# Kernel optimization log

Hardware: AMD Instinct MI355X
Metric: run time of the kernel (lower is better)

Reference implementation:

```python
import jax, jax.numpy as jnp
import numpy as np

NUM_HEADS = 16

def setup_inputs() -> dict:
    key = jax.random.key(0)
    ks = jax.random.split(key, 7)
    B, Q, K, D = 4, 512, 4096, 1024
    return {
        'query':  jax.random.normal(ks[0], (B, Q, D), dtype=jnp.float32),
        'memory': jax.random.normal(ks[1], (B, K, D), dtype=jnp.float32),
        'bias':   jax.random.normal(ks[2], (B, K), dtype=jnp.float32),
        'Wq': jax.random.normal(ks[3], (D, D), dtype=jnp.float32) * (D ** -0.5),
        'Wk': jax.random.normal(ks[4], (D, D), dtype=jnp.float32) * (D ** -0.5),
        'Wv': jax.random.normal(ks[5], (D, D), dtype=jnp.float32) * (D ** -0.5),
        'Wo': jax.random.normal(ks[6], (D, D), dtype=jnp.float32) * (D ** -0.5),
    }

def reference(query, memory, bias, Wq, Wk, Wv, Wo):
    B, Qn, _ = query.shape
    _, Kn, _ = memory.shape
    H = NUM_HEADS
    E = Wq.shape[1]
    dh = E // H
    scale = dh ** -0.5
    # projections (bias-free linears), split heads: [B, H, len, dh]
    q = (query @ Wq).reshape(B, Qn, H, dh).transpose(0, 2, 1, 3)
    k = (memory @ Wk).reshape(B, Kn, H, dh).transpose(0, 2, 1, 3)
    v = (memory @ Wv).reshape(B, Kn, H, dh).transpose(0, 2, 1, 3)
    scores = jnp.einsum('bhqd,bhkd->bhqk', q, k) * scale
    scores = scores + bias[:, None, None, :]          # additive support bias over K
    weights = jax.nn.softmax(scores, axis=-1)          # dropout p=0.0 -> identity
    out = jnp.einsum('bhqk,bhkd->bhqd', weights, v)
    out = out.transpose(0, 2, 1, 3).reshape(B, Qn, E)
    return out @ Wo
```

## Files before the change

### kernel.cpp

```cpp
#include <hip/hip_runtime.h>

typedef __attribute__((ext_vector_type(8))) short bf16x8;
typedef __attribute__((ext_vector_type(4))) short bf16x4;
typedef __attribute__((ext_vector_type(4))) float f32x4;

#define MFMA32(a,b,c) __builtin_amdgcn_mfma_f32_16x16x32_bf16((a),(b),(c),0,0,0)
#define MFMA16(a,b,c) __builtin_amdgcn_mfma_f32_16x16x16bf16_1k((a),(b),(c),0,0,0)
#define LOG2E 1.44269504f

#define BAR() asm volatile("s_barrier" ::: "memory")
#define VMW_(n) asm volatile("s_waitcnt vmcnt(" #n ")" ::: "memory")
#define VMW(n) VMW_(n)

__device__ __forceinline__ unsigned short f2bf(float f) {
  unsigned int u = __float_as_uint(f);
  u += 0x7fffu + ((u >> 16) & 1u);
  return (unsigned short)(u >> 16);
}

__device__ __forceinline__ void cp16(const void* g, void* l) {
  __builtin_amdgcn_global_load_lds((const __attribute__((address_space(1))) void*)g,
                                   (__attribute__((address_space(3))) void*)l, 16, 0, 0);
}

__global__ void conv_both(const float* __restrict__ q, const float* __restrict__ m,
                          const float* __restrict__ bias,
                          unsigned short* __restrict__ qo, unsigned short* __restrict__ mo,
                          float* __restrict__ bz) {
  int i = blockIdx.x * 256 + threadIdx.x;
  if (i < 524288) {
    float4 v = ((const float4*)q)[i];
    ushort4 o; o.x = f2bf(v.x); o.y = f2bf(v.y); o.z = f2bf(v.z); o.w = f2bf(v.w);
    ((ushort4*)qo)[i] = o;
  } else if (i < 4718592) {
    int j = i - 524288;
    float4 v = ((const float4*)m)[j];
    ushort4 o; o.x = f2bf(v.x); o.y = f2bf(v.y); o.z = f2bf(v.z); o.w = f2bf(v.w);
    ((ushort4*)mo)[j] = o;
  } else {
    int j = i - 4718592;
    float4 v = ((const float4*)bias)[j];
    float4 o;
    o.x = __builtin_fmaf(v.x, LOG2E, -16.f);
    o.y = __builtin_fmaf(v.y, LOG2E, -16.f);
    o.z = __builtin_fmaf(v.z, LOG2E, -16.f);
    o.w = __builtin_fmaf(v.w, LOG2E, -16.f);
    ((float4*)bz)[j] = o;
  }
}

__global__ void transpose4(const float* __restrict__ Wq, const float* __restrict__ Wk,
                           const float* __restrict__ Wv, const float* __restrict__ Wo,
                           unsigned short* __restrict__ dst) {
  __shared__ float t[32][33];
  int z = blockIdx.z;
  const float* W = (z == 0) ? Wq : (z == 1) ? Wk : (z == 2) ? Wv : Wo;
  unsigned short* WT = dst + (size_t)z * 1048576;
  int bx = blockIdx.x * 32, by = blockIdx.y * 32;
  int x = threadIdx.x, y0 = threadIdx.y;
#pragma unroll
  for (int r = 0; r < 4; ++r)
    t[y0 + r * 8][x] = W[(size_t)(by + y0 + r * 8) * 1024 + bx + x];
  __syncthreads();
#pragma unroll
  for (int r = 0; r < 4; ++r)
    WT[(size_t)(bx + y0 + r * 8) * 1024 + by + x] = f2bf(t[x][y0 + r * 8]);
}

__global__ __launch_bounds__(512, 2) void gemm_kv(
    const unsigned short* __restrict__ A,
    const unsigned short* __restrict__ Bk,
    const unsigned short* __restrict__ Bv,
    unsigned short* __restrict__ Kp,
    unsigned short* __restrict__ Vt)
{
  __shared__ __attribute__((aligned(16))) unsigned short lds[65536];
  const int tid = threadIdx.x;
  const int w = tid >> 6, lane = tid & 63;
  const int lh = lane & 15, q4 = lane >> 4;
  const int id = blockIdx.x;
  const int xcd = id & 7, j = id >> 3;
  const int tm = (xcd * 8 + (j >> 3)) * 256;
  const int tn = (j & 7) * 128;
  const int wm = (w >> 1) * 64, wn = (w & 1) * 64;

  const int r8 = lane >> 3;
  const int scol = ((lane & 7) ^ r8) * 8;
  const int srow = w * 8 + r8;
  const int fs0 = ((0 + q4) ^ (lh & 7)) * 8;
  const int fs1 = ((4 + q4) ^ (lh & 7)) * 8;

  const unsigned short* Ag = A  + (size_t)tm * 1024 + scol;
  const unsigned short* Kg = Bk + (size_t)tn * 1024 + scol;
  const unsigned short* Vg = Bv + (size_t)tn * 1024 + scol;

#define STG_A(BUF,KT,I) cp16(Ag + (size_t)((I)*64 + srow) * 1024 + (KT)*64, \
                             lds + (BUF)*32768 + (I)*4096 + w*512)
#define STG_K(BUF,KT,I) cp16(Kg + (size_t)((I)*64 + srow) * 1024 + (KT)*64, \
                             lds + (BUF)*32768 + 16384 + (I)*4096 + w*512)
#define STG_V(BUF,KT,I) cp16(Vg + (size_t)((I)*64 + srow) * 1024 + (KT)*64, \
                             lds + (BUF)*32768 + 24576 + (I)*4096 + w*512)

  f32x4 acck[4][4] = {}, accv[4][4] = {};
  bf16x8 aE[4], aO[4], bP[4], bQ[4];

  STG_A(0, 0, 0); STG_A(0, 0, 1); STG_A(0, 0, 2); STG_A(0, 0, 3);
  STG_K(0, 0, 0); STG_K(0, 0, 1);
  STG_V(0, 0, 0); STG_V(0, 0, 1);
  STG_A(1, 1, 0); STG_A(1, 1, 1); STG_A(1, 1, 2); STG_A(1, 1, 3);
  VMW(6);
  BAR();
#pragma unroll
  for (int m = 0; m < 4; ++m)
    aE[m] = *(const bf16x8*)(lds + (wm + m * 16 + lh) * 64 + fs0);
#pragma unroll
  for (int n = 0; n < 4; ++n)
    bP[n] = *(const bf16x8*)(lds + 16384 + (wn + n * 16 + lh) * 64 + fs0);

#define KV_TILE(CURB, TP1, TP2, DO_SB, DO_SA, VM1N, VM3N, DO_V3, DO_RDN)      \
  {                                                                           \
    const unsigned short* bse = lds + (CURB) * 32768;                         \
    const unsigned short* bnx = lds + ((CURB) ^ 1) * 32768;                   \
    const int nx = (CURB) ^ 1;                                                \
                            \
    BAR();                                                                    \
    _Pragma("unroll") for (int m = 0; m < 4; ++m)                             \
      aO[m] = *(const bf16x8*)(bse + (wm + m * 16 + lh) * 64 + fs1);          \
    _Pragma("unroll") for (int n = 0; n < 4; ++n)                             \
      bQ[n] = *(const bf16x8*)(bse + 16384 + (wn + n * 16 + lh) * 64 + fs1);  \
    if (DO_SB) { STG_K(nx, TP1, 0); STG_K(nx, TP1, 1); }                      \
    __builtin_amdgcn_s_setprio(1);                                            \
    _Pragma("unroll") for (int m = 0; m < 4; ++m)                             \
      _Pragma("unroll") for (int n = 0; n < 4; ++n)                           \
        acck[m][n] = MFMA32(aE[m], bP[n], acck[m][n]);                        \
    __builtin_amdgcn_s_setprio(0);                                            \
                      \
    VMW(VM1N);                                                                \
    BAR();                                                                    \
    _Pragma("unroll") for (int n = 0; n < 4; ++n)                             \
      bP[n] = *(const bf16x8*)(bse + 24576 + (wn + n * 16 + lh) * 64 + fs0);  \
    if (DO_SB) { STG_V(nx, TP1, 0); STG_V(nx, TP1, 1); }                      \
    __builtin_amdgcn_s_setprio(1);                                            \
    _Pragma("unroll") for (int m = 0; m < 4; ++m)                             \
      _Pragma("unroll") for (int n = 0; n < 4; ++n)                           \
        acck[m][n] = MFMA32(aO[m], bQ[n], acck[m][n]);                        \
    __builtin_amdgcn_s_setprio(0);                                            \
                         \
    BAR();                                                                    \
    _Pragma("unroll") for (int n = 0; n < 4; ++n)                             \
      bQ[n] = *(const bf16x8*)(bse + 24576 + (wn + n * 16 + lh) * 64 + fs1);  \
    if (DO_SA) { STG_A(CURB, TP2, 0); STG_A(CURB, TP2, 1); }                  \
    __builtin_amdgcn_s_setprio(1);                                            \
    _Pragma("unroll") for (int m = 0; m < 4; ++m)                             \
      _Pragma("unroll") for (int n = 0; n < 4; ++n)                           \
        accv[m][n] = MFMA32(aE[m], bP[n], accv[m][n]);                        \
    __builtin_amdgcn_s_setprio(0);                                            \
                   \
    if (DO_V3) { VMW(VM3N); }                                                 \
    BAR();                                                                    \
    if (DO_RDN) {                                                             \
      _Pragma("unroll") for (int m = 0; m < 4; ++m)                           \
        aE[m] = *(const bf16x8*)(bnx + (wm + m * 16 + lh) * 64 + fs0);        \
      _Pragma("unroll") for (int n = 0; n < 4; ++n)                           \
        bP[n] = *(const bf16x8*)(bnx + 16384 + (wn + n * 16 + lh) * 64 + fs0);\
    }                                                                         \
    if (DO_SA) { STG_A(CURB, TP2, 2); STG_A(CURB, TP2, 3); }                  \
    __builtin_amdgcn_s_setprio(1);                                            \
    _Pragma("unroll") for (int m = 0; m < 4; ++m)                             \
      _Pragma("unroll") for (int n = 0; n < 4; ++n)                           \
        accv[m][n] = MFMA32(aO[m], bQ[n], accv[m][n]);                        \
    __builtin_amdgcn_s_setprio(0);                                            \
  }

  for (int t = 0; t < 14; ++t) {
    KV_TILE(t & 1, t + 1, t + 2, 1, 1, 6, 4, 1, 1);
  }
  KV_TILE(0, 15, 16, 1, 0, 6, 2, 1, 1);
  KV_TILE(1, 16, 17, 0, 0, 0, 0, 0, 0);

#undef KV_TILE
#undef STG_A
#undef STG_K
#undef STG_V

#pragma unroll
  for (int m = 0; m < 4; ++m)
#pragma unroll
    for (int n = 0; n < 4; ++n) {
      int row = tm + wm + m * 16 + q4 * 4;
      int col = tn + wn + n * 16 + lh;
#pragma unroll
      for (int e = 0; e < 4; ++e)
        Kp[(size_t)(row + e) * 1024 + col] = f2bf(acck[m][n][e]);
    }

  __syncthreads();
#pragma unroll
  for (int m = 0; m < 4; ++m)
#pragma unroll
    for (int n = 0; n < 4; ++n) {
      int row = wm + m * 16 + q4 * 4;
      int col = wn + n * 16 + lh;
      ushort4 v4;
      v4.x = f2bf(accv[m][n][0]); v4.y = f2bf(accv[m][n][1]);
      v4.z = f2bf(accv[m][n][2]); v4.w = f2bf(accv[m][n][3]);
      *(ushort4*)(lds + col * 256 + (row ^ ((col & 31) << 3))) = v4;
    }
  __syncthreads();
#pragma unroll
  for (int p = 0; p < 8; ++p) {
    int col = p * 16 + (tid >> 5);
    int jb = tid & 31;
    const unsigned short* src = lds + col * 256 + ((jb ^ (col & 31)) << 3);
    *(int4*)(Vt + (size_t)(tn + col) * 16384 + tm + jb * 8) = *(const int4*)src;
  }
}

__global__ __launch_bounds__(256) void gemm_bt64(
    const unsigned short* __restrict__ A, const unsigned short* __restrict__ B,
    float* __restrict__ Cf, unsigned short* __restrict__ Cb,
    int M, int N, int K, float scale)
{
  __shared__ __attribute__((aligned(16))) unsigned short lds[6144];
  int w = threadIdx.x >> 6, lane = threadIdx.x & 63;
  int lh = lane & 15, q4 = lane >> 4;
  int tm = blockIdx.y * 128, tn = blockIdx.x * 64;
  int wm = (w & 1) * 64, wn = (w >> 1) * 32;

  int srow = lane >> 2;
  int scol = ((lane & 3) ^ ((lane >> 3) & 3)) << 3;
  int q4s = (q4 ^ ((lh >> 1) & 3)) << 3;

  f32x4 acc[4][2] = {};

  for (int k0 = 0; k0 < K; k0 += 32) {
#pragma unroll
    for (int i = 0; i < 2; ++i) {
      int c = w * 2 + i;
      int row = c * 16 + srow;
      cp16(A + (size_t)(tm + row) * K + k0 + scol, lds + c * 512);
    }
    {
      int row = w * 16 + srow;
      cp16(B + (size_t)(tn + row) * K + k0 + scol, lds + 4096 + w * 512);
    }
    __syncthreads();
    bf16x8 afr[4], bfr[2];
#pragma unroll
    for (int r = 0; r < 4; ++r)
      afr[r] = *(const bf16x8*)(lds + (wm + r * 16 + lh) * 32 + q4s);
#pragma unroll
    for (int c = 0; c < 2; ++c)
      bfr[c] = *(const bf16x8*)(lds + 4096 + (wn + c * 16 + lh) * 32 + q4s);
#pragma unroll
    for (int r = 0; r < 4; ++r)
#pragma unroll
      for (int c = 0; c < 2; ++c)
        acc[r][c] = MFMA32(afr[r], bfr[c], acc[r][c]);
    __syncthreads();
  }

#pragma unroll
  for (int r = 0; r < 4; ++r)
#pragma unroll
    for (int c = 0; c < 2; ++c)
#pragma unroll
      for (int e = 0; e < 4; ++e) {
        int row = tm + wm + r * 16 + q4 * 4 + e;
        int col = tn + wn + c * 16 + lh;
        if (Cb) Cb[(size_t)row * N + col] = f2bf(acc[r][c][e] * scale);
        else    Cf[(size_t)row * N + col] = acc[r][c][e] * scale;
      }
}

__global__ __launch_bounds__(256) void attn_kernel(
    const unsigned short* __restrict__ Q, const unsigned short* __restrict__ Kp,
    const unsigned short* __restrict__ VT, const float* __restrict__ bz,
    float* __restrict__ po, float* __restrict__ lp)
{
  __shared__ __attribute__((aligned(16))) unsigned short Klds[4096];
  __shared__ __attribute__((aligned(16))) unsigned short Vlds[4096];
  int w = threadIdx.x >> 6, lane = threadIdx.x & 63;
  int lh = lane & 15, q4 = lane >> 4;

  int id = blockIdx.x;
  int xcd = id & 7, j = id >> 3;
  int ql = j & 7;
  int half = ql & 1, qt = ql >> 1;
  int bh = (j >> 3) * 8 + xcd;
  int b = bh >> 4, h = bh & 15;
  int q0 = qt * 128;
  int t00 = half * 2048;

  const unsigned short* Qb = Q + (size_t)(b * 512 + q0 + w * 32) * 1024 + h * 64;
  const unsigned short* Kb = Kp + (size_t)(b * 4096) * 1024 + h * 64;
  const unsigned short* Vb = VT + (size_t)(h * 64) * 16384 + b * 4096;
  const float* bzg = bz + (size_t)b * 4096;

  bf16x8 bq[2][2];
#pragma unroll
  for (int s = 0; s < 2; ++s)
#pragma unroll
    for (int th = 0; th < 2; ++th)
      bq[s][th] = *(const bf16x8*)(Qb + (size_t)(s * 16 + lh) * 1024 + th * 32 + q4 * 8);

  f32x4 oa[2][4] = {};
  float ls[2] = {0.f, 0.f};

  int rl = lane >> 3, blk = lane & 7;
  int sw = ((blk ^ rl) * 8);

  for (int ti = 0; ti < 32; ++ti) {
    int t = t00 + ti * 64;
#pragma unroll
    for (int r = 0; r < 2; ++r) {
      int seg = r * 4 + w;
      int row = seg * 8 + rl;
      cp16(Kb + (size_t)(t + row) * 1024 + sw, Klds + seg * 512);
      cp16(Vb + (size_t)row * 16384 + t + sw, Vlds + seg * 512);
    }
    __syncthreads();

    float4 bz4[4];
#pragma unroll
    for (int c = 0; c < 4; ++c)
      bz4[c] = *(const float4*)(bzg + t + c * 16 + q4 * 4);

    bf16x8 kf[4][2];
#pragma unroll
    for (int c = 0; c < 4; ++c)
#pragma unroll
      for (int th = 0; th < 2; ++th)
        kf[c][th] = *(const bf16x8*)(Klds + (c * 16 + lh) * 64 + (((th << 2) + q4) ^ (lh & 7)) * 8);
    bf16x4 vf[4][4];
#pragma unroll
    for (int c = 0; c < 4; ++c)
#pragma unroll
      for (int c2 = 0; c2 < 4; ++c2)
        vf[c][c2] = *(const bf16x4*)(Vlds + (c2 * 16 + lh) * 64 +
                                     (((c << 1) + (q4 >> 1)) ^ (lh & 7)) * 8 + (q4 & 1) * 4);

#pragma unroll
    for (int s = 0; s < 2; ++s) {
#pragma unroll
      for (int c = 0; c < 4; ++c) {
        f32x4 z = {};
        z = MFMA32(kf[c][0], bq[s][0], z);
        z = MFMA32(kf[c][1], bq[s][1], z);
        float bzf[4] = {bz4[c].x, bz4[c].y, bz4[c].z, bz4[c].w};
        bf16x4 pb;
        float ps = 0.f;
#pragma unroll
        for (int e = 0; e < 4; ++e) {
          float p = __builtin_amdgcn_exp2f(z[e] + bzf[e]);
          ps += p;
          pb[e] = (short)f2bf(p);
        }
        ls[s] += ps;
#pragma unroll
        for (int c2 = 0; c2 < 4; ++c2)
          oa[s][c2] = MFMA16(vf[c][c2], pb, oa[s][c2]);
      }
    }
    __syncthreads();
  }

#pragma unroll
  for (int s = 0; s < 2; ++s) {
    ls[s] += __shfl_xor(ls[s], 16);
    ls[s] += __shfl_xor(ls[s], 32);
  }

  int sl = bh * 4 + qt;
  float* pslice = po + (size_t)(half * 256 + sl) * 8192;
#pragma unroll
  for (int s = 0; s < 2; ++s) {
    if (q4 == 0) lp[half * 32768 + sl * 128 + w * 32 + s * 16 + lh] = ls[s];
#pragma unroll
    for (int c2 = 0; c2 < 4; ++c2)
#pragma unroll
      for (int e = 0; e < 4; ++e)
        pslice[(c2 * 16 + q4 * 4 + e) * 128 + w * 32 + s * 16 + lh] = oa[s][c2][e];
  }
}

__global__ void norm_kernel(const float* __restrict__ po, const float* __restrict__ lp,
                            unsigned short* __restrict__ ao) {
  int g = blockIdx.x * 256 + threadIdx.x;
  int d8 = (g & 7) * 8;
  int rowid = g >> 3;
  int bh = rowid >> 9, rq = rowid & 511, qt = rq >> 7, qcol = rq & 127;
  int sl = bh * 4 + qt;
  const float* p0 = po + (size_t)sl * 8192;
  const float* p1 = po + (size_t)(256 + sl) * 8192;
  float l = lp[sl * 128 + qcol] + lp[32768 + sl * 128 + qcol];
  float inv = 1.f / l;
  unsigned short o8[8];
#pragma unroll
  for (int k = 0; k < 8; ++k)
    o8[k] = f2bf((p0[(d8 + k) * 128 + qcol] + p1[(d8 + k) * 128 + qcol]) * inv);
  int b = bh >> 4, h = bh & 15;
  unsigned short* dst = ao + (size_t)(b * 512 + qt * 128 + qcol) * 1024 + h * 64 + d8;
  *(ushort4*)dst = *(ushort4*)o8;
  *(ushort4*)(dst + 4) = *(ushort4*)(o8 + 4);
}

extern "C" void kernel_launch(void* const* d_in, const int* in_sizes, int n_in,
                              void* d_out, int out_size, void* d_ws, size_t ws_size,
                              hipStream_t stream) {
  const float* query  = (const float*)d_in[0];
  const float* memory = (const float*)d_in[1];
  const float* bias   = (const float*)d_in[2];
  const float* Wq     = (const float*)d_in[3];
  const float* Wk     = (const float*)d_in[4];
  const float* Wv     = (const float*)d_in[5];
  const float* Wo     = (const float*)d_in[6];
  float* out = (float*)d_out;

  unsigned short* ws  = (unsigned short*)d_ws;
  unsigned short* qbf = ws;
  unsigned short* mbf = qbf + 2097152;
  unsigned short* WqT = mbf + 16777216;
  unsigned short* WkT = WqT + 1048576;
  unsigned short* WvT = WkT + 1048576;
  unsigned short* WoT = WvT + 1048576;
  unsigned short* qp  = WoT + 1048576;
  unsigned short* kp  = qp + 2097152;
  unsigned short* vT  = kp + 16777216;
  unsigned short* ao  = vT + 16777216;
  float* bzw = (float*)(ao + 2097152);
  float* po = (float*)ws;
  float* lp = po + 4194304;

  conv_both<<<18448, 256, 0, stream>>>(query, memory, bias, qbf, mbf, bzw);
  transpose4<<<dim3(32, 32, 4), dim3(32, 8), 0, stream>>>(Wq, Wk, Wv, Wo, WqT);

  gemm_bt64<<<dim3(16, 16), 256, 0, stream>>>(qbf, WqT, nullptr, qp, 2048, 1024, 1024, 0.125f * LOG2E);
  gemm_kv<<<512, 512, 0, stream>>>(mbf, WkT, WvT, kp, vT);

  attn_kernel<<<512, 256, 0, stream>>>(qp, kp, vT, bzw, po, lp);
  norm_kernel<<<1024, 256, 0, stream>>>(po, lp, ao);

  gemm_bt64<<<dim3(16, 16), 256, 0, stream>>>(ao, WoT, out, nullptr, 2048, 1024, 1024, 1.f);
}
```

Baseline: 304.4 us.

## Double-buffer gemm_bt64 and simplify the KV projection pipeline to one barrier per tile

The output/Q projection GEMM gets a second LDS buffer. The next K-slice is now prefetched right after a single barrier at the top of each step, so the trailing barrier goes away and loads overlap the MFMAs. The KV projection kernel drops its hand-staggered macro schedule, with its split loads, custom waitcnts and raw s_barrier. In its place is a plain double-buffered loop that loads the whole next tile, then runs the K and V MFMAs in two k-halves. This is simpler, but the generic __syncthreads may wait on all outstanding loads, which could expose memory latency the old finer-grained schedule hid.

Measured after the change: 289.7 us. -4.8%, faster.

```diff
diff --git a/kernel.cpp b/kernel.cpp
--- a/kernel.cpp
+++ b/kernel.cpp
@@ -7,10 +7,6 @@
 #define MFMA32(a,b,c) __builtin_amdgcn_mfma_f32_16x16x32_bf16((a),(b),(c),0,0,0)
 #define MFMA16(a,b,c) __builtin_amdgcn_mfma_f32_16x16x16bf16_1k((a),(b),(c),0,0,0)
 #define LOG2E 1.44269504f
-
-#define BAR() asm volatile("s_barrier" ::: "memory")
-#define VMW_(n) asm volatile("s_waitcnt vmcnt(" #n ")" ::: "memory")
-#define VMW(n) VMW_(n)
 
 __device__ __forceinline__ unsigned short f2bf(float f) {
   unsigned int u = __float_as_uint(f);
@@ -102,83 +98,63 @@
                              lds + (BUF)*32768 + 24576 + (I)*4096 + w*512)
 
   f32x4 acck[4][4] = {}, accv[4][4] = {};
-  bf16x8 aE[4], aO[4], bP[4], bQ[4];
 
   STG_A(0, 0, 0); STG_A(0, 0, 1); STG_A(0, 0, 2); STG_A(0, 0, 3);
   STG_K(0, 0, 0); STG_K(0, 0, 1);
   STG_V(0, 0, 0); STG_V(0, 0, 1);
-  STG_A(1, 1, 0); STG_A(1, 1, 1); STG_A(1, 1, 2); STG_A(1, 1, 3);
-  VMW(6);
-  BAR();
-#pragma unroll
-  for (int m = 0; m < 4; ++m)
-    aE[m] = *(const bf16x8*)(lds + (wm + m * 16 + lh) * 64 + fs0);
-#pragma unroll
-  for (int n = 0; n < 4; ++n)
-    bP[n] = *(const bf16x8*)(lds + 16384 + (wn + n * 16 + lh) * 64 + fs0);
-
-#define KV_TILE(CURB, TP1, TP2, DO_SB, DO_SA, VM1N, VM3N, DO_V3, DO_RDN)      \
-  {                                                                           \
-    const unsigned short* bse = lds + (CURB) * 32768;                         \
-    const unsigned short* bnx = lds + ((CURB) ^ 1) * 32768;                   \
-    const int nx = (CURB) ^ 1;                                                \
-                            \
-    BAR();                                                                    \
-    _Pragma("unroll") for (int m = 0; m < 4; ++m)                             \
-      aO[m] = *(const bf16x8*)(bse + (wm + m * 16 + lh) * 64 + fs1);          \
-    _Pragma("unroll") for (int n = 0; n < 4; ++n)                             \
-      bQ[n] = *(const bf16x8*)(bse + 16384 + (wn + n * 16 + lh) * 64 + fs1);  \
-    if (DO_SB) { STG_K(nx, TP1, 0); STG_K(nx, TP1, 1); }                      \
-    __builtin_amdgcn_s_setprio(1);                                            \
-    _Pragma("unroll") for (int m = 0; m < 4; ++m)                             \
-      _Pragma("unroll") for (int n = 0; n < 4; ++n)                           \
-        acck[m][n] = MFMA32(aE[m], bP[n], acck[m][n]);                        \
-    __builtin_amdgcn_s_setprio(0);                                            \
-                      \
-    VMW(VM1N);                                                                \
-    BAR();                                                                    \
-    _Pragma("unroll") for (int n = 0; n < 4; ++n)                             \
-      bP[n] = *(const bf16x8*)(bse + 24576 + (wn + n * 16 + lh) * 64 + fs0);  \
-    if (DO_SB) { STG_V(nx, TP1, 0); STG_V(nx, TP1, 1); }                      \
-    __builtin_amdgcn_s_setprio(1);                                            \
-    _Pragma("unroll") for (int m = 0; m < 4; ++m)                             \
-      _Pragma("unroll") for (int n = 0; n < 4; ++n)                           \
-        acck[m][n] = MFMA32(aO[m], bQ[n], acck[m][n]);                        \
-    __builtin_amdgcn_s_setprio(0);                                            \
-                         \
-    BAR();                                                                    \
-    _Pragma("unroll") for (int n = 0; n < 4; ++n)                             \
-      bQ[n] = *(const bf16x8*)(bse + 24576 + (wn + n * 16 + lh) * 64 + fs1);  \
-    if (DO_SA) { STG_A(CURB, TP2, 0); STG_A(CURB, TP2, 1); }                  \
-    __builtin_amdgcn_s_setprio(1);                                            \
-    _Pragma("unroll") for (int m = 0; m < 4; ++m)                             \
-      _Pragma("unroll") for (int n = 0; n < 4; ++n)                           \
-        accv[m][n] = MFMA32(aE[m], bP[n], accv[m][n]);                        \
-    __builtin_amdgcn_s_setprio(0);                                            \
-                   \
-    if (DO_V3) { VMW(VM3N); }                                                 \
-    BAR();                                                                    \
-    if (DO_RDN) {                                                             \
-      _Pragma("unroll") for (int m = 0; m < 4; ++m)                           \
-        aE[m] = *(const bf16x8*)(bnx + (wm + m * 16 + lh) * 64 + fs0);        \
-      _Pragma("unroll") for (int n = 0; n < 4; ++n)                           \
-        bP[n] = *(const bf16x8*)(bnx + 16384 + (wn + n * 16 + lh) * 64 + fs0);\
-    }                                                                         \
-    if (DO_SA) { STG_A(CURB, TP2, 2); STG_A(CURB, TP2, 3); }                  \
-    __builtin_amdgcn_s_setprio(1);                                            \
-    _Pragma("unroll") for (int m = 0; m < 4; ++m)                             \
-      _Pragma("unroll") for (int n = 0; n < 4; ++n)                           \
-        accv[m][n] = MFMA32(aO[m], bQ[n], accv[m][n]);                        \
-    __builtin_amdgcn_s_setprio(0);                                            \
-  }
-
-  for (int t = 0; t < 14; ++t) {
-    KV_TILE(t & 1, t + 1, t + 2, 1, 1, 6, 4, 1, 1);
-  }
-  KV_TILE(0, 15, 16, 1, 0, 6, 2, 1, 1);
-  KV_TILE(1, 16, 17, 0, 0, 0, 0, 0, 0);
-
-#undef KV_TILE
+
+  for (int t = 0; t < 16; ++t) {
+    const unsigned short* bse = lds + (t & 1) * 32768;
+    const int nx = (t & 1) ^ 1;
+    __syncthreads();
+    if (t < 15) {
+      STG_A(nx, t + 1, 0); STG_A(nx, t + 1, 1);
+      STG_A(nx, t + 1, 2); STG_A(nx, t + 1, 3);
+      STG_K(nx, t + 1, 0); STG_K(nx, t + 1, 1);
+      STG_V(nx, t + 1, 0); STG_V(nx, t + 1, 1);
+    }
+    {
+      bf16x8 a0[4], bk0[4], bv0[4];
+#pragma unroll
+      for (int m = 0; m < 4; ++m)
+        a0[m] = *(const bf16x8*)(bse + (wm + m * 16 + lh) * 64 + fs0);
+#pragma unroll
+      for (int n = 0; n < 4; ++n) {
+        bk0[n] = *(const bf16x8*)(bse + 16384 + (wn + n * 16 + lh) * 64 + fs0);
+        bv0[n] = *(const bf16x8*)(bse + 24576 + (wn + n * 16 + lh) * 64 + fs0);
+      }
+      __builtin_amdgcn_s_setprio(1);
+#pragma unroll
+      for (int m = 0; m < 4; ++m)
+#pragma unroll
+        for (int n = 0; n < 4; ++n) {
+          acck[m][n] = MFMA32(a0[m], bk0[n], acck[m][n]);
+          accv[m][n] = MFMA32(a0[m], bv0[n], accv[m][n]);
+        }
+      __builtin_amdgcn_s_setprio(0);
+    }
+    {
+      bf16x8 a1[4], bk1[4], bv1[4];
+#pragma unroll
+      for (int m = 0; m < 4; ++m)
+        a1[m] = *(const bf16x8*)(bse + (wm + m * 16 + lh) * 64 + fs1);
+#pragma unroll
+      for (int n = 0; n < 4; ++n) {
+        bk1[n] = *(const bf16x8*)(bse + 16384 + (wn + n * 16 + lh) * 64 + fs1);
+        bv1[n] = *(const bf16x8*)(bse + 24576 + (wn + n * 16 + lh) * 64 + fs1);
+      }
+      __builtin_amdgcn_s_setprio(1);
+#pragma unroll
+      for (int m = 0; m < 4; ++m)
+#pragma unroll
+        for (int n = 0; n < 4; ++n) {
+          acck[m][n] = MFMA32(a1[m], bk1[n], acck[m][n]);
+          accv[m][n] = MFMA32(a1[m], bv1[n], accv[m][n]);
+        }
+      __builtin_amdgcn_s_setprio(0);
+    }
+  }
+
 #undef STG_A
 #undef STG_K
 #undef STG_V
@@ -221,7 +197,7 @@
     float* __restrict__ Cf, unsigned short* __restrict__ Cb,
     int M, int N, int K, float scale)
 {
-  __shared__ __attribute__((aligned(16))) unsigned short lds[6144];
+  __shared__ __attribute__((aligned(16))) unsigned short lds[12288];
   int w = threadIdx.x >> 6, lane = threadIdx.x & 63;
   int lh = lane & 15, q4 = lane >> 4;
   int tm = blockIdx.y * 128, tn = blockIdx.x * 64;
@@ -231,34 +207,42 @@
   int scol = ((lane & 3) ^ ((lane >> 3) & 3)) << 3;
   int q4s = (q4 ^ ((lh >> 1) & 3)) << 3;
 
+#define STG64(BUF,K0)                                                          \
+  {                                                                            \
+    _Pragma("unroll") for (int i = 0; i < 2; ++i) {                            \
+      int c = w * 2 + i;                                                       \
+      cp16(A + (size_t)(tm + c * 16 + srow) * K + (K0) + scol,                 \
+           lds + (BUF) * 6144 + c * 512);                                      \
+    }                                                                          \
+    cp16(B + (size_t)(tn + w * 16 + srow) * K + (K0) + scol,                   \
+         lds + (BUF) * 6144 + 4096 + w * 512);                                 \
+  }
+
   f32x4 acc[4][2] = {};
-
-  for (int k0 = 0; k0 < K; k0 += 32) {
-#pragma unroll
-    for (int i = 0; i < 2; ++i) {
-      int c = w * 2 + i;
-      int row = c * 16 + srow;
-      cp16(A + (size_t)(tm + row) * K + k0 + scol, lds + c * 512);
-    }
-    {
-      int row = w * 16 + srow;
-      cp16(B + (size_t)(tn + row) * K + k0 + scol, lds + 4096 + w * 512);
-    }
+  const int nst = K >> 5;
+
+  STG64(0, 0);
+
+  for (int t = 0; t < nst; ++t) {
+    const unsigned short* bse = lds + (t & 1) * 6144;
     __syncthreads();
+    if (t + 1 < nst) STG64((t & 1) ^ 1, (t + 1) << 5);
     bf16x8 afr[4], bfr[2];
 #pragma unroll
     for (int r = 0; r < 4; ++r)
-      afr[r] = *(const bf16x8*)(lds + (wm + r * 16 + lh) * 32 + q4s);
+      afr[r] = *(const bf16x8*)(bse + (wm + r * 16 + lh) * 32 + q4s);
 #pragma unroll
     for (int c = 0; c < 2; ++c)
-      bfr[c] = *(const bf16x8*)(lds + 4096 + (wn + c * 16 + lh) * 32 + q4s);
+      bfr[c] = *(const bf16x8*)(bse + 4096 + (wn + c * 16 + lh) * 32 + q4s);
+    __builtin_amdgcn_s_setprio(1);
 #pragma unroll
     for (int r = 0; r < 4; ++r)
 #pragma unroll
       for (int c = 0; c < 2; ++c)
         acc[r][c] = MFMA32(afr[r], bfr[c], acc[r][c]);
-    __syncthreads();
-  }
+    __builtin_amdgcn_s_setprio(0);
+  }
+#undef STG64
 
 #pragma unroll
   for (int r = 0; r < 4; ++r)
```
